# Optimization experiments

Measured on AMD Instinct MI355X. Metric: run time of the kernel, lower is better.

Reference implementation:

```python
import jax, jax.numpy as jnp
import numpy as np

H = 51  # hidden size hardcoded in the module


def _lstm_cell(x, h, c, W_ih, b_ih, W_hh, b_hh):
    # PyTorch LSTMCell: gates in i, f, g, o order
    gates = x @ W_ih.T + b_ih + h @ W_hh.T + b_hh  # [B, 4H]
    i, f, g, o = jnp.split(gates, 4, axis=-1)
    i = jax.nn.sigmoid(i)
    f = jax.nn.sigmoid(f)
    g = jnp.tanh(g)
    o = jax.nn.sigmoid(o)
    c_new = f * c + i * g
    h_new = o * jnp.tanh(c_new)
    return h_new, c_new


def setup_inputs() -> dict:
    key = jax.random.key(0)
    ks = jax.random.split(key, 12)
    B, T = 2048, 256
    s1 = 1.0 / np.sqrt(H)
    u = lambda k, shape: jax.random.uniform(k, shape, jnp.float32, -s1, s1)
    return {
        "inputs": jax.random.normal(ks[0], (B, T), jnp.float32),
        "W_ih1": u(ks[1], (4 * H, 1)),
        "b_ih1": u(ks[2], (4 * H,)),
        "W_hh1": u(ks[3], (4 * H, H)),
        "b_hh1": u(ks[4], (4 * H,)),
        "W_ih2": u(ks[5], (4 * H, H)),
        "b_ih2": u(ks[6], (4 * H,)),
        "W_hh2": u(ks[7], (4 * H, H)),
        "b_hh2": u(ks[8], (4 * H,)),
        "W_lin": u(ks[9], (1, H)),
        "b_lin": u(ks[10], (1,)),
        "future": 16,
    }


def reference(inputs, W_ih1, b_ih1, W_hh1, b_hh1, W_ih2, b_ih2, W_hh2, b_hh2,
              W_lin, b_lin, future):
    B, T = inputs.shape
    h1 = jnp.zeros((B, H), inputs.dtype)
    c1 = jnp.zeros((B, H), inputs.dtype)
    h2 = jnp.zeros((B, H), inputs.dtype)
    c2 = jnp.zeros((B, H), inputs.dtype)

    def core(x_t, h1, c1, h2, c2):
        h1, c1 = _lstm_cell(x_t, h1, c1, W_ih1, b_ih1, W_hh1, b_hh1)
        h2, c2 = _lstm_cell(h1, h2, c2, W_ih2, b_ih2, W_hh2, b_hh2)
        out = h2 @ W_lin.T + b_lin  # [B, 1]
        return out, h1, c1, h2, c2

    def step(carry, x_t):
        h1, c1, h2, c2, _ = carry
        out, h1, c1, h2, c2 = core(x_t, h1, c1, h2, c2)
        return (h1, c1, h2, c2, out), out

    xs = inputs.T[:, :, None]  # [T, B, 1]
    init_out = jnp.zeros((B, 1), inputs.dtype)
    carry, outs_seen = jax.lax.scan(step, (h1, c1, h2, c2, init_out), xs)

    def fstep(carry, _):
        h1, c1, h2, c2, out = carry
        out, h1, c1, h2, c2 = core(out, h1, c1, h2, c2)
        return (h1, c1, h2, c2, out), out

    if future > 0:
        _, outs_fut = jax.lax.scan(fstep, carry, None, length=future)
        outs = jnp.concatenate([outs_seen, outs_fut], axis=0)  # [T+F, B, 1]
    else:
        outs = outs_seen
    return outs[:, :, 0].T  # [B, T+future]
```

## Files before the change

### kernel.cpp

```cpp
#include <hip/hip_runtime.h>
#include <math.h>

#define H 51
#define TSEEN 256
#define FUT 16
#define TTOT (TSEEN + FUT)
#define NB 8
#define THREADS 512
#define NWAVE 8
#define UPW 7
#define NBLOCKS (2048 / NB)

typedef _Float16 f16;
typedef _Float16 f16x8 __attribute__((ext_vector_type(8)));
typedef float f32x4 __attribute__((ext_vector_type(4)));

__device__ __forceinline__ float fast_rcp(float x) { return __builtin_amdgcn_rcpf(x); }
__device__ __forceinline__ float sigf(float x) {
  return fast_rcp(1.f + __expf(-x));
}
__device__ __forceinline__ float tanhf_(float x) {
  return fmaf(2.f, fast_rcp(1.f + __expf(-2.f * x)), -1.f);
}

__device__ __forceinline__ float xor8f(float v) {
  return __int_as_float(__builtin_amdgcn_mov_dpp(__float_as_int(v), 0x128, 0xf, 0xf, true));
}

#define MFMA __builtin_amdgcn_mfma_f32_16x16x32_f16

__device__ __forceinline__ void recomb(const f32x4& a0, const f32x4& a1, bool mhi,
                                       float& q0, float& q1, float& q2, float& q3) {
  float s0 = mhi ? a0[0] : a1[0];
  float s1 = mhi ? a0[1] : a1[1];
  float s2 = mhi ? a0[2] : a1[2];
  float s3 = mhi ? a0[3] : a1[3];
  float k0 = mhi ? a1[0] : a0[0];
  float k1 = mhi ? a1[1] : a0[1];
  float k2 = mhi ? a1[2] : a0[2];
  float k3 = mhi ? a1[3] : a0[3];
  q0 = k0 + xor8f(s0);
  q1 = k1 + xor8f(s1);
  q2 = k2 + xor8f(s2);
  q3 = k3 + xor8f(s3);
}

__launch_bounds__(THREADS, 2)
__global__ void lstm2_kernel(const float* __restrict__ inp,
                             const float* __restrict__ Wih1,
                             const float* __restrict__ bih1,
                             const float* __restrict__ Whh1,
                             const float* __restrict__ bhh1,
                             const float* __restrict__ Wih2,
                             const float* __restrict__ bih2,
                             const float* __restrict__ Whh2,
                             const float* __restrict__ bhh2,
                             const float* __restrict__ Wlin,
                             const float* __restrict__ blin,
                             float* __restrict__ out)
{
  __shared__ __align__(16) f16 Bh1[2][2][64][8];
  __shared__ __align__(16) f16 Bh2[2][2][64][8];
  __shared__ __align__(16) float xs[TSEEN][NB];
  __shared__ float parts[2][NWAVE][NB];
  __shared__ float outb[TTOT][NB];

  const int tid  = threadIdx.x;
  const int wv   = tid >> 6;
  const int lane = tid & 63;
  const int l15  = lane & 15;
  const int g4   = lane >> 4;
  const int bq   = l15 & 7;
  const bool mhi = (l15 & 8) != 0;
  const int baseb = blockIdx.x * NB;

  {
    f16* b1 = &Bh1[0][0][0][0];
    f16* b2 = &Bh2[0][0][0][0];
    for (int i = tid; i < 2 * 2 * 64 * 8; i += THREADS) {
      b1[i] = (f16)0.f; b2[i] = (f16)0.f;
    }
  }
  for (int i = tid; i < NB * TSEEN; i += THREADS) {
    int b = i >> 8, t = i & 255;
    xs[t][b] = inp[(size_t)(baseb + b) * TSEEN + t];
  }
  if (tid < 2 * NWAVE * NB) (&parts[0][0][0])[tid] = 0.f;

  f16x8 A1[2][2], A2[2][2], A3[2][2];
  #pragma unroll
  for (int m = 0; m < 2; ++m) {
    const int slotA = 4 * m + (l15 >> 2);
    const int uA = UPW * wv + slotA;
    const int gA = l15 & 3;
    const bool vA = (slotA < UPW) && (uA < H);
    const int row = gA * H + (vA ? uA : 0);
    #pragma unroll
    for (int kt = 0; kt < 2; ++kt) {
      #pragma unroll
      for (int j = 0; j < 8; ++j) {
        const int k = 32 * kt + 8 * g4 + j;
        float w1 = 0.f, w2 = 0.f, w3 = 0.f;
        if (vA) {
          if (k < H) {
            w1 = Whh1[row * H + k];
            w2 = Wih2[row * H + k];
            w3 = Whh2[row * H + k];
          } else if (k == H) {
            w1 = Wih1[row];
          }
        }
        A1[m][kt][j] = (f16)w1;
        A2[m][kt][j] = (f16)w2;
        A3[m][kt][j] = (f16)w3;
      }
    }
  }

  f32x4 bias1[2], bias2[2];
  #pragma unroll
  for (int m = 0; m < 2; ++m) {
    const int ulC = 4 * m + g4;
    const int u = UPW * wv + ulC;
    const bool v = (ulC < UPW) && (u < H) && (l15 < 8);
    #pragma unroll
    for (int r = 0; r < 4; ++r) {
      const int rr = r * H + (v ? u : 0);
      bias1[m][r] = v ? (bih1[rr] + bhh1[rr]) : 0.f;
      bias2[m][r] = v ? (bih2[rr] + bhh2[rr]) : 0.f;
    }
  }

  const int slotC = (mhi ? 4 : 0) + g4;
  const int uC0 = UPW * wv + slotC;
  const bool vC = (slotC < UPW) && (uC0 < H);
  const int uC = vC ? uC0 : 0;
  const float wl = vC ? Wlin[uC] : 0.f;
  const float bl = blin[0];
  const int wkt = uC >> 5;
  const int wln = bq + 16 * ((uC >> 3) & 3);
  const int wj  = uC & 7;

  float c1 = 0.f, c2 = 0.f;
  const f32x4 zf = {0.f, 0.f, 0.f, 0.f};

  __syncthreads();
  if (tid < NB) {
    float x0 = xs[0][tid];
    f16 xh = (f16)x0;
    Bh1[1][1][tid + 32][3] = xh;
    Bh1[1][1][tid + 40][3] = (f16)(x0 - (float)xh);
  }
  __syncthreads();

  f32x4 ac1[2];
  {
    const f16x8 p0 = *(const f16x8*)&Bh1[1][0][lane][0];
    const f16x8 p1 = *(const f16x8*)&Bh1[1][1][lane][0];
    #pragma unroll
    for (int m = 0; m < 2; ++m) {
      f32x4 c = MFMA(A1[m][0], p0, bias1[m], 0, 0, 0);
      ac1[m] = MFMA(A1[m][1], p1, c, 0, 0, 0);
    }
  }

  #pragma unroll 1
  for (int t = 0; t < TTOT; ++t) {
    const int pw = t & 1, pr = pw ^ 1;

    float q0, q1, q2, q3;
    recomb(ac1[0], ac1[1], mhi, q0, q1, q2, q3);
    {
      float iv = sigf(q0), fv = sigf(q1);
      float gv = tanhf_(q2), ov = sigf(q3);
      c1 = fmaf(fv, c1, iv * gv);
      float h1n = ov * tanhf_(c1);
      if (vC) {
        f16 hh = (f16)h1n;
        Bh1[pw][wkt][wln][wj]     = hh;
        Bh1[pw][wkt][wln + 8][wj] = (f16)(h1n - (float)hh);
      }
    }
    if (t + 1 < TSEEN && tid < NB) {
      float xn = xs[t + 1][tid];
      f16 xh = (f16)xn;
      Bh1[pw][1][tid + 32][3] = xh;
      Bh1[pw][1][tid + 40][3] = (f16)(xn - (float)xh);
    }
    __syncthreads();

    if (t >= 1 && t < TSEEN && tid < NB) {
      float s = bl;
      #pragma unroll
      for (int w = 0; w < NWAVE; ++w) s += parts[pr][w][tid];
      outb[t - 1][tid] = s;
    }

    const f16x8 b2k0 = *(const f16x8*)&Bh2[pr][0][lane][0];
    const f16x8 b2k1 = *(const f16x8*)&Bh2[pr][1][lane][0];
    const f16x8 f1k0 = *(const f16x8*)&Bh1[pw][0][lane][0];
    const f16x8 f1k1 = *(const f16x8*)&Bh1[pw][1][lane][0];

    f32x4 ac2[2];
    #pragma unroll
    for (int m = 0; m < 2; ++m) {
      f32x4 r1 = MFMA(A3[m][0], b2k0, bias2[m], 0, 0, 0);
      r1 = MFMA(A3[m][1], b2k1, r1, 0, 0, 0);
      f32x4 r2 = MFMA(A2[m][0], f1k0, zf, 0, 0, 0);
      r2 = MFMA(A2[m][1], f1k1, r2, 0, 0, 0);
      ac2[m] = r1 + r2;
      f32x4 n = MFMA(A1[m][0], f1k0, bias1[m], 0, 0, 0);
      ac1[m] = MFMA(A1[m][1], f1k1, n, 0, 0, 0);
    }

    recomb(ac2[0], ac2[1], mhi, q0, q1, q2, q3);
    float pv;
    {
      float iv = sigf(q0), fv = sigf(q1);
      float gv = tanhf_(q2), ov = sigf(q3);
      c2 = fmaf(fv, c2, iv * gv);
      float h2n = ov * tanhf_(c2);
      pv = wl * h2n;
      if (vC) {
        f16 hh = (f16)h2n;
        Bh2[pw][wkt][wln][wj]     = hh;
        Bh2[pw][wkt][wln + 8][wj] = (f16)(h2n - (float)hh);
      }
    }
    pv += xor8f(pv);
    pv += __shfl_xor(pv, 16, 64);
    pv += __shfl_xor(pv, 32, 64);
    if (lane < NB) parts[pw][wv][lane] = pv;

    if (t >= TSEEN - 1) {
      __syncthreads();
      if (tid < NB) {
        float fbv = bl;
        #pragma unroll
        for (int w = 0; w < NWAVE; ++w) fbv += parts[pw][w][tid];
        outb[t][tid] = fbv;
        if (t < TTOT - 1) {
          f16 xh = (f16)fbv;
          Bh1[pw][1][tid + 32][3] = xh;
          Bh1[pw][1][tid + 40][3] = (f16)(fbv - (float)xh);
        }
      }
      __syncthreads();
      if (t < TTOT - 1) {
        const f16x8 g0 = *(const f16x8*)&Bh1[pw][0][lane][0];
        const f16x8 g1 = *(const f16x8*)&Bh1[pw][1][lane][0];
        #pragma unroll
        for (int m = 0; m < 2; ++m) {
          f32x4 c = MFMA(A1[m][0], g0, bias1[m], 0, 0, 0);
          ac1[m] = MFMA(A1[m][1], g1, c, 0, 0, 0);
        }
      }
    }
  }

  __syncthreads();
  for (int i = tid; i < TTOT * NB; i += THREADS) {
    int b = i / TTOT, t = i - b * TTOT;
    out[(size_t)(baseb + b) * TTOT + t] = outb[t][b];
  }
}

extern "C" void kernel_launch(void* const* d_in, const int* in_sizes, int n_in,
                              void* d_out, int out_size, void* d_ws, size_t ws_size,
                              hipStream_t stream) {
  (void)in_sizes; (void)n_in; (void)d_ws; (void)ws_size; (void)out_size;
  const float* inp  = (const float*)d_in[0];
  const float* Wih1 = (const float*)d_in[1];
  const float* bih1 = (const float*)d_in[2];
  const float* Whh1 = (const float*)d_in[3];
  const float* bhh1 = (const float*)d_in[4];
  const float* Wih2 = (const float*)d_in[5];
  const float* bih2 = (const float*)d_in[6];
  const float* Whh2 = (const float*)d_in[7];
  const float* bhh2 = (const float*)d_in[8];
  const float* Wlin = (const float*)d_in[9];
  const float* blin = (const float*)d_in[10];
  float* outp = (float*)d_out;

  lstm2_kernel<<<NBLOCKS, THREADS, 0, stream>>>(
      inp, Wih1, bih1, Whh1, bhh1, Wih2, bih2, Whh2, bhh2, Wlin, blin, outp);
}
```

Baseline: 231.0 us.

## Spread hidden units across 16 waves with one MFMA tile per wave

Doubles the block to 1024 threads (16 waves), so each wave owns 3–4 hidden units and a single 16-row MFMA tile instead of two tiles plus a cross-tile recombine. The per-step serial chain per wave gets shorter (fewer MFMAs, no select-based recombine), and the cross-wave output partials are stored transposed so they can be summed with vector loads. In exchange each block barrier now spans more waves, and the launch bound asks for 4 blocks per CU, which tightens the register budget.

```diff
diff --git a/kernel.cpp b/kernel.cpp
--- a/kernel.cpp
+++ b/kernel.cpp
@@ -6,9 +6,8 @@
 #define FUT 16
 #define TTOT (TSEEN + FUT)
 #define NB 8
-#define THREADS 512
-#define NWAVE 8
-#define UPW 7
+#define THREADS 1024
+#define NWAVE 16
 #define NBLOCKS (2048 / NB)
 
 typedef _Float16 f16;
@@ -29,23 +28,7 @@
 
 #define MFMA __builtin_amdgcn_mfma_f32_16x16x32_f16
 
-__device__ __forceinline__ void recomb(const f32x4& a0, const f32x4& a1, bool mhi,
-                                       float& q0, float& q1, float& q2, float& q3) {
-  float s0 = mhi ? a0[0] : a1[0];
-  float s1 = mhi ? a0[1] : a1[1];
-  float s2 = mhi ? a0[2] : a1[2];
-  float s3 = mhi ? a0[3] : a1[3];
-  float k0 = mhi ? a1[0] : a0[0];
-  float k1 = mhi ? a1[1] : a0[1];
-  float k2 = mhi ? a1[2] : a0[2];
-  float k3 = mhi ? a1[3] : a0[3];
-  q0 = k0 + xor8f(s0);
-  q1 = k1 + xor8f(s1);
-  q2 = k2 + xor8f(s2);
-  q3 = k3 + xor8f(s3);
-}
-
-__launch_bounds__(THREADS, 2)
+__launch_bounds__(THREADS, 4)
 __global__ void lstm2_kernel(const float* __restrict__ inp,
                              const float* __restrict__ Wih1,
                              const float* __restrict__ bih1,
@@ -62,7 +45,7 @@
   __shared__ __align__(16) f16 Bh1[2][2][64][8];
   __shared__ __align__(16) f16 Bh2[2][2][64][8];
   __shared__ __align__(16) float xs[TSEEN][NB];
-  __shared__ float parts[2][NWAVE][NB];
+  __shared__ __align__(16) float parts[2][NB][NWAVE];
   __shared__ float outb[TTOT][NB];
 
   const int tid  = threadIdx.x;
@@ -71,8 +54,10 @@
   const int l15  = lane & 15;
   const int g4   = lane >> 4;
   const int bq   = l15 & 7;
-  const bool mhi = (l15 & 8) != 0;
   const int baseb = blockIdx.x * NB;
+
+  const int ubase = (51 * wv) >> 4;
+  const int ucnt  = ((51 * (wv + 1)) >> 4) - ubase;
 
   {
     f16* b1 = &Bh1[0][0][0][0];
@@ -85,16 +70,15 @@
     int b = i >> 8, t = i & 255;
     xs[t][b] = inp[(size_t)(baseb + b) * TSEEN + t];
   }
-  if (tid < 2 * NWAVE * NB) (&parts[0][0][0])[tid] = 0.f;
-
-  f16x8 A1[2][2], A2[2][2], A3[2][2];
-  #pragma unroll
-  for (int m = 0; m < 2; ++m) {
-    const int slotA = 4 * m + (l15 >> 2);
-    const int uA = UPW * wv + slotA;
+  if (tid < 2 * NB * NWAVE) (&parts[0][0][0])[tid] = 0.f;
+
+  f16x8 A1[2], A2[2], A3[2];
+  {
+    const int slotA = l15 >> 2;
     const int gA = l15 & 3;
-    const bool vA = (slotA < UPW) && (uA < H);
-    const int row = gA * H + (vA ? uA : 0);
+    const bool vA = (slotA < ucnt);
+    const int uA = ubase + (vA ? slotA : 0);
+    const int row = gA * H + uA;
     #pragma unroll
     for (int kt = 0; kt < 2; ++kt) {
       #pragma unroll
@@ -110,31 +94,27 @@
             w1 = Wih1[row];
           }
         }
-        A1[m][kt][j] = (f16)w1;
-        A2[m][kt][j] = (f16)w2;
-        A3[m][kt][j] = (f16)w3;
-      }
-    }
-  }
-
-  f32x4 bias1[2], bias2[2];
-  #pragma unroll
-  for (int m = 0; m < 2; ++m) {
-    const int ulC = 4 * m + g4;
-    const int u = UPW * wv + ulC;
-    const bool v = (ulC < UPW) && (u < H) && (l15 < 8);
+        A1[kt][j] = (f16)w1;
+        A2[kt][j] = (f16)w2;
+        A3[kt][j] = (f16)w3;
+      }
+    }
+  }
+
+  f32x4 bias1, bias2;
+  {
+    const bool vb = (g4 < ucnt) && (l15 < 8);
+    const int ucb = ubase + ((g4 < ucnt) ? g4 : 0);
     #pragma unroll
     for (int r = 0; r < 4; ++r) {
-      const int rr = r * H + (v ? u : 0);
-      bias1[m][r] = v ? (bih1[rr] + bhh1[rr]) : 0.f;
-      bias2[m][r] = v ? (bih2[rr] + bhh2[rr]) : 0.f;
-    }
-  }
-
-  const int slotC = (mhi ? 4 : 0) + g4;
-  const int uC0 = UPW * wv + slotC;
-  const bool vC = (slotC < UPW) && (uC0 < H);
-  const int uC = vC ? uC0 : 0;
+      const int rr = r * H + ucb;
+      bias1[r] = vb ? (bih1[rr] + bhh1[rr]) : 0.f;
+      bias2[r] = vb ? (bih2[rr] + bhh2[rr]) : 0.f;
+    }
+  }
+
+  const bool vC = (g4 < ucnt) && (l15 < 8);
+  const int uC = ubase + ((g4 < ucnt) ? g4 : 0);
   const float wl = vC ? Wlin[uC] : 0.f;
   const float bl = blin[0];
   const int wkt = uC >> 5;
@@ -153,23 +133,22 @@
   }
   __syncthreads();
 
-  f32x4 ac1[2];
+  f32x4 ac1;
   {
     const f16x8 p0 = *(const f16x8*)&Bh1[1][0][lane][0];
     const f16x8 p1 = *(const f16x8*)&Bh1[1][1][lane][0];
-    #pragma unroll
-    for (int m = 0; m < 2; ++m) {
-      f32x4 c = MFMA(A1[m][0], p0, bias1[m], 0, 0, 0);
-      ac1[m] = MFMA(A1[m][1], p1, c, 0, 0, 0);
-    }
+    f32x4 c = MFMA(A1[0], p0, bias1, 0, 0, 0);
+    ac1 = MFMA(A1[1], p1, c, 0, 0, 0);
   }
 
   #pragma unroll 1
   for (int t = 0; t < TTOT; ++t) {
     const int pw = t & 1, pr = pw ^ 1;
 
-    float q0, q1, q2, q3;
-    recomb(ac1[0], ac1[1], mhi, q0, q1, q2, q3);
+    float q0 = ac1[0] + xor8f(ac1[0]);
+    float q1 = ac1[1] + xor8f(ac1[1]);
+    float q2 = ac1[2] + xor8f(ac1[2]);
+    float q3 = ac1[3] + xor8f(ac1[3]);
     {
       float iv = sigf(q0), fv = sigf(q1);
       float gv = tanhf_(q2), ov = sigf(q3);
@@ -190,9 +169,12 @@
     __syncthreads();
 
     if (t >= 1 && t < TSEEN && tid < NB) {
-      float s = bl;
-      #pragma unroll
-      for (int w = 0; w < NWAVE; ++w) s += parts[pr][w][tid];
+      const float4 pa = *(const float4*)&parts[pr][tid][0];
+      const float4 pb = *(const float4*)&parts[pr][tid][4];
+      const float4 pc = *(const float4*)&parts[pr][tid][8];
+      const float4 pd = *(const float4*)&parts[pr][tid][12];
+      float s = bl + (((pa.x + pa.y) + (pa.z + pa.w)) + ((pb.x + pb.y) + (pb.z + pb.w)))
+                   + (((pc.x + pc.y) + (pc.z + pc.w)) + ((pd.x + pd.y) + (pd.z + pd.w)));
       outb[t - 1][tid] = s;
     }
 
@@ -201,19 +183,20 @@
     const f16x8 f1k0 = *(const f16x8*)&Bh1[pw][0][lane][0];
     const f16x8 f1k1 = *(const f16x8*)&Bh1[pw][1][lane][0];
 
-    f32x4 ac2[2];
-    #pragma unroll
-    for (int m = 0; m < 2; ++m) {
-      f32x4 r1 = MFMA(A3[m][0], b2k0, bias2[m], 0, 0, 0);
-      r1 = MFMA(A3[m][1], b2k1, r1, 0, 0, 0);
-      f32x4 r2 = MFMA(A2[m][0], f1k0, zf, 0, 0, 0);
-      r2 = MFMA(A2[m][1], f1k1, r2, 0, 0, 0);
-      ac2[m] = r1 + r2;
-      f32x4 n = MFMA(A1[m][0], f1k0, bias1[m], 0, 0, 0);
-      ac1[m] = MFMA(A1[m][1], f1k1, n, 0, 0, 0);
-    }
-
-    recomb(ac2[0], ac2[1], mhi, q0, q1, q2, q3);
+    f32x4 r1 = MFMA(A3[0], b2k0, bias2, 0, 0, 0);
+    r1 = MFMA(A3[1], b2k1, r1, 0, 0, 0);
+    f32x4 r2 = MFMA(A2[0], f1k0, zf, 0, 0, 0);
+    r2 = MFMA(A2[1], f1k1, r2, 0, 0, 0);
+    f32x4 ac2 = r1 + r2;
+    {
+      f32x4 n = MFMA(A1[0], f1k0, bias1, 0, 0, 0);
+      ac1 = MFMA(A1[1], f1k1, n, 0, 0, 0);
+    }
+
+    q0 = ac2[0] + xor8f(ac2[0]);
+    q1 = ac2[1] + xor8f(ac2[1]);
+    q2 = ac2[2] + xor8f(ac2[2]);
+    q3 = ac2[3] + xor8f(ac2[3]);
     float pv;
     {
       float iv = sigf(q0), fv = sigf(q1);
@@ -227,17 +210,19 @@
         Bh2[pw][wkt][wln + 8][wj] = (f16)(h2n - (float)hh);
       }
     }
-    pv += xor8f(pv);
     pv += __shfl_xor(pv, 16, 64);
     pv += __shfl_xor(pv, 32, 64);
-    if (lane < NB) parts[pw][wv][lane] = pv;
+    if (lane < NB) parts[pw][lane][wv] = pv;
 
     if (t >= TSEEN - 1) {
       __syncthreads();
       if (tid < NB) {
-        float fbv = bl;
-        #pragma unroll
-        for (int w = 0; w < NWAVE; ++w) fbv += parts[pw][w][tid];
+        const float4 pa = *(const float4*)&parts[pw][tid][0];
+        const float4 pb = *(const float4*)&parts[pw][tid][4];
+        const float4 pc = *(const float4*)&parts[pw][tid][8];
+        const float4 pd = *(const float4*)&parts[pw][tid][12];
+        float fbv = bl + (((pa.x + pa.y) + (pa.z + pa.w)) + ((pb.x + pb.y) + (pb.z + pb.w)))
+                       + (((pc.x + pc.y) + (pc.z + pc.w)) + ((pd.x + pd.y) + (pd.z + pd.w)));
         outb[t][tid] = fbv;
         if (t < TTOT - 1) {
           f16 xh = (f16)fbv;
@@ -249,11 +234,8 @@
       if (t < TTOT - 1) {
         const f16x8 g0 = *(const f16x8*)&Bh1[pw][0][lane][0];
         const f16x8 g1 = *(const f16x8*)&Bh1[pw][1][lane][0];
-        #pragma unroll
-        for (int m = 0; m < 2; ++m) {
-          f32x4 c = MFMA(A1[m][0], g0, bias1[m], 0, 0, 0);
-          ac1[m] = MFMA(A1[m][1], g1, c, 0, 0, 0);
-        }
+        f32x4 c = MFMA(A1[0], g0, bias1, 0, 0, 0);
+        ac1 = MFMA(A1[1], g1, c, 0, 0, 0);
       }
     }
   }
```

Measured after the change: 297.4 us. +28.7%, slower.

## Split LSTM units across 4 waves of 16 instead of 8 waves of 7

Applied to the files above, without the earlier changes.

Each block now runs 4 waves instead of 8, and each wave handles 16 hidden units as four MFMA row tiles. Every lane computes the gate math for two units instead of one. The aim is cheaper per-step block barriers and a shorter cross-wave reduction of the output partials. In exchange, each wave issues twice as many MFMAs and activations per timestep on the serial recurrence path, and the block has fewer waves to hide latency.

```diff
diff --git a/kernel.cpp b/kernel.cpp
--- a/kernel.cpp
+++ b/kernel.cpp
@@ -6,9 +6,8 @@
 #define FUT 16
 #define TTOT (TSEEN + FUT)
 #define NB 8
-#define THREADS 512
-#define NWAVE 8
-#define UPW 7
+#define THREADS 256
+#define NWAVE 4
 #define NBLOCKS (2048 / NB)
 
 typedef _Float16 f16;
@@ -29,23 +28,7 @@
 
 #define MFMA __builtin_amdgcn_mfma_f32_16x16x32_f16
 
-__device__ __forceinline__ void recomb(const f32x4& a0, const f32x4& a1, bool mhi,
-                                       float& q0, float& q1, float& q2, float& q3) {
-  float s0 = mhi ? a0[0] : a1[0];
-  float s1 = mhi ? a0[1] : a1[1];
-  float s2 = mhi ? a0[2] : a1[2];
-  float s3 = mhi ? a0[3] : a1[3];
-  float k0 = mhi ? a1[0] : a0[0];
-  float k1 = mhi ? a1[1] : a0[1];
-  float k2 = mhi ? a1[2] : a0[2];
-  float k3 = mhi ? a1[3] : a0[3];
-  q0 = k0 + xor8f(s0);
-  q1 = k1 + xor8f(s1);
-  q2 = k2 + xor8f(s2);
-  q3 = k3 + xor8f(s3);
-}
-
-__launch_bounds__(THREADS, 2)
+__launch_bounds__(THREADS, 1)
 __global__ void lstm2_kernel(const float* __restrict__ inp,
                              const float* __restrict__ Wih1,
                              const float* __restrict__ bih1,
@@ -87,13 +70,13 @@
   }
   if (tid < 2 * NWAVE * NB) (&parts[0][0][0])[tid] = 0.f;
 
-  f16x8 A1[2][2], A2[2][2], A3[2][2];
+  f16x8 A1[4][2], A2[4][2], A3[4][2];
   #pragma unroll
-  for (int m = 0; m < 2; ++m) {
-    const int slotA = 4 * m + (l15 >> 2);
-    const int uA = UPW * wv + slotA;
+  for (int m = 0; m < 4; ++m) {
+    const int slotA = l15 >> 2;
     const int gA = l15 & 3;
-    const bool vA = (slotA < UPW) && (uA < H);
+    const int uA = 16 * wv + 4 * m + slotA;
+    const bool vA = (uA < H);
     const int row = gA * H + (vA ? uA : 0);
     #pragma unroll
     for (int kt = 0; kt < 2; ++kt) {
@@ -117,48 +100,48 @@
     }
   }
 
-  f32x4 bias1[2], bias2[2];
+  f32x4 bias1[4], bias2[4];
   #pragma unroll
-  for (int m = 0; m < 2; ++m) {
-    const int ulC = 4 * m + g4;
-    const int u = UPW * wv + ulC;
-    const bool v = (ulC < UPW) && (u < H) && (l15 < 8);
+  for (int m = 0; m < 4; ++m) {
+    const int ub = 16 * wv + 4 * m + g4;
+    const bool vb = (ub < H) && (l15 < 8);
     #pragma unroll
     for (int r = 0; r < 4; ++r) {
-      const int rr = r * H + (v ? u : 0);
-      bias1[m][r] = v ? (bih1[rr] + bhh1[rr]) : 0.f;
-      bias2[m][r] = v ? (bih2[rr] + bhh2[rr]) : 0.f;
-    }
-  }
-
-  const int slotC = (mhi ? 4 : 0) + g4;
-  const int uC0 = UPW * wv + slotC;
-  const bool vC = (slotC < UPW) && (uC0 < H);
-  const int uC = vC ? uC0 : 0;
-  const float wl = vC ? Wlin[uC] : 0.f;
+      const int rr = r * H + (vb ? ub : 0);
+      bias1[m][r] = vb ? (bih1[rr] + bhh1[rr]) : 0.f;
+      bias2[m][r] = vb ? (bih2[rr] + bhh2[rr]) : 0.f;
+    }
+  }
+
+  const int tA = mhi ? 2 : 0, tB = mhi ? 3 : 1;
+  const int uCA0 = 16 * wv + 4 * tA + g4;
+  const int uCB0 = 16 * wv + 4 * tB + g4;
+  const bool vCA = (uCA0 < H), vCB = (uCB0 < H);
+  const int uCA = vCA ? uCA0 : 0, uCB = vCB ? uCB0 : 0;
+  const float wlA = vCA ? Wlin[uCA] : 0.f;
+  const float wlB = vCB ? Wlin[uCB] : 0.f;
   const float bl = blin[0];
-  const int wkt = uC >> 5;
-  const int wln = bq + 16 * ((uC >> 3) & 3);
-  const int wj  = uC & 7;
-
-  float c1 = 0.f, c2 = 0.f;
+  const int wktA = uCA >> 5, wlnA = bq + 16 * ((uCA >> 3) & 3), wjA = uCA & 7;
+  const int wktB = uCB >> 5, wlnB = bq + 16 * ((uCB >> 3) & 3), wjB = uCB & 7;
+
+  float c1A = 0.f, c1B = 0.f, c2A = 0.f, c2B = 0.f;
   const f32x4 zf = {0.f, 0.f, 0.f, 0.f};
 
   __syncthreads();
-  if (tid < NB) {
-    float x0 = xs[0][tid];
+  if (lane < NB && wv == 0) {
+    float x0 = xs[0][lane];
     f16 xh = (f16)x0;
-    Bh1[1][1][tid + 32][3] = xh;
-    Bh1[1][1][tid + 40][3] = (f16)(x0 - (float)xh);
+    Bh1[1][1][lane + 32][3] = xh;
+    Bh1[1][1][lane + 40][3] = (f16)(x0 - (float)xh);
   }
   __syncthreads();
 
-  f32x4 ac1[2];
+  f32x4 ac1[4];
   {
     const f16x8 p0 = *(const f16x8*)&Bh1[1][0][lane][0];
     const f16x8 p1 = *(const f16x8*)&Bh1[1][1][lane][0];
     #pragma unroll
-    for (int m = 0; m < 2; ++m) {
+    for (int m = 0; m < 4; ++m) {
       f32x4 c = MFMA(A1[m][0], p0, bias1[m], 0, 0, 0);
       ac1[m] = MFMA(A1[m][1], p1, c, 0, 0, 0);
     }
@@ -168,32 +151,48 @@
   for (int t = 0; t < TTOT; ++t) {
     const int pw = t & 1, pr = pw ^ 1;
 
-    float q0, q1, q2, q3;
-    recomb(ac1[0], ac1[1], mhi, q0, q1, q2, q3);
+    float qA0, qA1, qA2, qA3, qB0, qB1, qB2, qB3;
     {
-      float iv = sigf(q0), fv = sigf(q1);
-      float gv = tanhf_(q2), ov = sigf(q3);
-      c1 = fmaf(fv, c1, iv * gv);
-      float h1n = ov * tanhf_(c1);
-      if (vC) {
-        f16 hh = (f16)h1n;
-        Bh1[pw][wkt][wln][wj]     = hh;
-        Bh1[pw][wkt][wln + 8][wj] = (f16)(h1n - (float)hh);
-      }
-    }
-    if (t + 1 < TSEEN && tid < NB) {
-      float xn = xs[t + 1][tid];
+      float s;
+      s = mhi ? ac1[0][0] : ac1[2][0]; qA0 = (mhi ? ac1[2][0] : ac1[0][0]) + xor8f(s);
+      s = mhi ? ac1[0][1] : ac1[2][1]; qA1 = (mhi ? ac1[2][1] : ac1[0][1]) + xor8f(s);
+      s = mhi ? ac1[0][2] : ac1[2][2]; qA2 = (mhi ? ac1[2][2] : ac1[0][2]) + xor8f(s);
+      s = mhi ? ac1[0][3] : ac1[2][3]; qA3 = (mhi ? ac1[2][3] : ac1[0][3]) + xor8f(s);
+      s = mhi ? ac1[1][0] : ac1[3][0]; qB0 = (mhi ? ac1[3][0] : ac1[1][0]) + xor8f(s);
+      s = mhi ? ac1[1][1] : ac1[3][1]; qB1 = (mhi ? ac1[3][1] : ac1[1][1]) + xor8f(s);
+      s = mhi ? ac1[1][2] : ac1[3][2]; qB2 = (mhi ? ac1[3][2] : ac1[1][2]) + xor8f(s);
+      s = mhi ? ac1[1][3] : ac1[3][3]; qB3 = (mhi ? ac1[3][3] : ac1[1][3]) + xor8f(s);
+    }
+    {
+      float ivA = sigf(qA0), fvA = sigf(qA1), gvA = tanhf_(qA2), ovA = sigf(qA3);
+      float ivB = sigf(qB0), fvB = sigf(qB1), gvB = tanhf_(qB2), ovB = sigf(qB3);
+      c1A = fmaf(fvA, c1A, ivA * gvA);
+      c1B = fmaf(fvB, c1B, ivB * gvB);
+      float h1A = ovA * tanhf_(c1A);
+      float h1B = ovB * tanhf_(c1B);
+      if (vCA) {
+        f16 hh = (f16)h1A;
+        Bh1[pw][wktA][wlnA][wjA]     = hh;
+        Bh1[pw][wktA][wlnA + 8][wjA] = (f16)(h1A - (float)hh);
+      }
+      if (vCB) {
+        f16 hh = (f16)h1B;
+        Bh1[pw][wktB][wlnB][wjB]     = hh;
+        Bh1[pw][wktB][wlnB + 8][wjB] = (f16)(h1B - (float)hh);
+      }
+    }
+    if (t + 1 < TSEEN && lane < NB) {
+      float xn = xs[t + 1][lane];
       f16 xh = (f16)xn;
-      Bh1[pw][1][tid + 32][3] = xh;
-      Bh1[pw][1][tid + 40][3] = (f16)(xn - (float)xh);
+      Bh1[pw][1][lane + 32][3] = xh;
+      Bh1[pw][1][lane + 40][3] = (f16)(xn - (float)xh);
     }
     __syncthreads();
 
-    if (t >= 1 && t < TSEEN && tid < NB) {
-      float s = bl;
-      #pragma unroll
-      for (int w = 0; w < NWAVE; ++w) s += parts[pr][w][tid];
-      outb[t - 1][tid] = s;
+    if (t >= 1 && t < TSEEN && lane < NB) {
+      float s = bl + parts[pr][0][lane] + parts[pr][1][lane]
+                   + parts[pr][2][lane] + parts[pr][3][lane];
+      outb[t - 1][lane] = s;
     }
 
     const f16x8 b2k0 = *(const f16x8*)&Bh2[pr][0][lane][0];
@@ -201,9 +200,9 @@
     const f16x8 f1k0 = *(const f16x8*)&Bh1[pw][0][lane][0];
     const f16x8 f1k1 = *(const f16x8*)&Bh1[pw][1][lane][0];
 
-    f32x4 ac2[2];
+    f32x4 ac2[4];
     #pragma unroll
-    for (int m = 0; m < 2; ++m) {
+    for (int m = 0; m < 4; ++m) {
       f32x4 r1 = MFMA(A3[m][0], b2k0, bias2[m], 0, 0, 0);
       r1 = MFMA(A3[m][1], b2k1, r1, 0, 0, 0);
       f32x4 r2 = MFMA(A2[m][0], f1k0, zf, 0, 0, 0);
@@ -213,18 +212,35 @@
       ac1[m] = MFMA(A1[m][1], f1k1, n, 0, 0, 0);
     }
 
-    recomb(ac2[0], ac2[1], mhi, q0, q1, q2, q3);
+    {
+      float s;
+      s = mhi ? ac2[0][0] : ac2[2][0]; qA0 = (mhi ? ac2[2][0] : ac2[0][0]) + xor8f(s);
+      s = mhi ? ac2[0][1] : ac2[2][1]; qA1 = (mhi ? ac2[2][1] : ac2[0][1]) + xor8f(s);
+      s = mhi ? ac2[0][2] : ac2[2][2]; qA2 = (mhi ? ac2[2][2] : ac2[0][2]) + xor8f(s);
+      s = mhi ? ac2[0][3] : ac2[2][3]; qA3 = (mhi ? ac2[2][3] : ac2[0][3]) + xor8f(s);
+      s = mhi ? ac2[1][0] : ac2[3][0]; qB0 = (mhi ? ac2[3][0] : ac2[1][0]) + xor8f(s);
+      s = mhi ? ac2[1][1] : ac2[3][1]; qB1 = (mhi ? ac2[3][1] : ac2[1][1]) + xor8f(s);
+      s = mhi ? ac2[1][2] : ac2[3][2]; qB2 = (mhi ? ac2[3][2] : ac2[1][2]) + xor8f(s);
+      s = mhi ? ac2[1][3] : ac2[3][3]; qB3 = (mhi ? ac2[3][3] : ac2[1][3]) + xor8f(s);
+    }
     float pv;
     {
-      float iv = sigf(q0), fv = sigf(q1);
-      float gv = tanhf_(q2), ov = sigf(q3);
-      c2 = fmaf(fv, c2, iv * gv);
-      float h2n = ov * tanhf_(c2);
-      pv = wl * h2n;
-      if (vC) {
-        f16 hh = (f16)h2n;
-        Bh2[pw][wkt][wln][wj]     = hh;
-        Bh2[pw][wkt][wln + 8][wj] = (f16)(h2n - (float)hh);
+      float ivA = sigf(qA0), fvA = sigf(qA1), gvA = tanhf_(qA2), ovA = sigf(qA3);
+      float ivB = sigf(qB0), fvB = sigf(qB1), gvB = tanhf_(qB2), ovB = sigf(qB3);
+      c2A = fmaf(fvA, c2A, ivA * gvA);
+      c2B = fmaf(fvB, c2B, ivB * gvB);
+      float h2A = ovA * tanhf_(c2A);
+      float h2B = ovB * tanhf_(c2B);
+      pv = fmaf(wlA, h2A, wlB * h2B);
+      if (vCA) {
+        f16 hh = (f16)h2A;
+        Bh2[pw][wktA][wlnA][wjA]     = hh;
+        Bh2[pw][wktA][wlnA + 8][wjA] = (f16)(h2A - (float)hh);
+      }
+      if (vCB) {
+        f16 hh = (f16)h2B;
+        Bh2[pw][wktB][wlnB][wjB]     = hh;
+        Bh2[pw][wktB][wlnB + 8][wjB] = (f16)(h2B - (float)hh);
       }
     }
     pv += xor8f(pv);
@@ -234,15 +250,14 @@
 
     if (t >= TSEEN - 1) {
       __syncthreads();
-      if (tid < NB) {
-        float fbv = bl;
-        #pragma unroll
-        for (int w = 0; w < NWAVE; ++w) fbv += parts[pw][w][tid];
-        outb[t][tid] = fbv;
+      if (lane < NB) {
+        float fbv = bl + parts[pw][0][lane] + parts[pw][1][lane]
+                      + parts[pw][2][lane] + parts[pw][3][lane];
+        outb[t][lane] = fbv;
         if (t < TTOT - 1) {
           f16 xh = (f16)fbv;
-          Bh1[pw][1][tid + 32][3] = xh;
-          Bh1[pw][1][tid + 40][3] = (f16)(fbv - (float)xh);
+          Bh1[pw][1][lane + 32][3] = xh;
+          Bh1[pw][1][lane + 40][3] = (f16)(fbv - (float)xh);
         }
       }
       __syncthreads();
@@ -250,7 +265,7 @@
         const f16x8 g0 = *(const f16x8*)&Bh1[pw][0][lane][0];
         const f16x8 g1 = *(const f16x8*)&Bh1[pw][1][lane][0];
         #pragma unroll
-        for (int m = 0; m < 2; ++m) {
+        for (int m = 0; m < 4; ++m) {
           f32x4 c = MFMA(A1[m][0], g0, bias1[m], 0, 0, 0);
           ac1[m] = MFMA(A1[m][1], g1, c, 0, 0, 0);
         }
```

Measured after the change: 309.0 us. 1.34x slower.
